# Kernel tuning notes

Hardware: AMD Instinct MI355X
Metric: run time of the kernel (lower is better)

## Reference

```python
import jax, jax.numpy as jnp
import numpy as np

B, N, T = 64, 256, 512          # batch, num_objs, num_triples
DO, DP, H, DOUT = 512, 512, 512, 512


def setup_inputs() -> dict:
    key = jax.random.key(0)
    ks = jax.random.split(key, 12)

    def kaiming(k, shape):
        fan_in = shape[0]
        return jax.random.normal(k, shape, jnp.float32) * np.sqrt(2.0 / fan_in)

    return {
        "obj_vecs": jax.random.normal(ks[0], (B, N, DO), jnp.float32),
        "pred_vecs": jax.random.normal(ks[1], (B, T, DP), jnp.float32),
        "edges": jax.random.randint(ks[2], (B, T, 3), 0, N, jnp.int64),
        # net1: [2*DO+DP -> H -> 2*H+DOUT], ReLU after each Linear
        "n1_w1": kaiming(ks[3], (2 * DO + DP, H)),
        "n1_b1": jnp.zeros((H,), jnp.float32),
        "n1_w2": kaiming(ks[4], (H, 2 * H + DOUT)),
        "n1_b2": jnp.zeros((2 * H + DOUT,), jnp.float32),
        # net2: [H -> H -> DOUT], ReLU after each Linear
        "n2_w1": kaiming(ks[5], (H, H)),
        "n2_b1": jnp.zeros((H,), jnp.float32),
        "n2_w2": kaiming(ks[6], (H, DOUT)),
        "n2_b2": jnp.zeros((DOUT,), jnp.float32),
    }


def reference(obj_vecs, pred_vecs, edges,
              n1_w1, n1_b1, n1_w2, n1_b2,
              n2_w1, n2_b1, n2_w2, n2_b2):
    num_batch, num_objs, _ = obj_vecs.shape
    h_dim = n1_b1.shape[0]
    d_out = n2_w2.shape[1]

    s_idx = edges[:, :, 0]            # [B, T] subject node ids
    o_idx = edges[:, :, 2]            # [B, T] object node ids

    # gather subject/object vectors per triple
    cur_s = jnp.take_along_axis(obj_vecs, s_idx[:, :, None], axis=1)  # [B,T,DO]
    cur_o = jnp.take_along_axis(obj_vecs, o_idx[:, :, None], axis=1)  # [B,T,DO]
    cur_t = jnp.concatenate([cur_s, pred_vecs, cur_o], axis=-1)       # [B,T,2DO+DP]

    # net1 MLP (Linear+ReLU, Linear+ReLU)
    hid = jax.nn.relu(jnp.einsum('btd,dh->bth', cur_t, n1_w1) + n1_b1)
    new_t = jax.nn.relu(jnp.einsum('bth,hk->btk', hid, n1_w2) + n1_b2)

    new_s = new_t[:, :, :h_dim]
    new_p = new_t[:, :, h_dim:h_dim + d_out]
    new_o = new_t[:, :, h_dim + d_out:2 * h_dim + d_out]

    # scatter-add back to nodes, per batch element
    b_ix = jnp.arange(num_batch)[:, None]            # [B,1]
    pooled = jnp.zeros((num_batch, num_objs, h_dim), obj_vecs.dtype)
    pooled = pooled.at[b_ix, s_idx].add(new_s)
    pooled = pooled.at[b_ix, o_idx].add(new_o)

    # avg pooling: divide by per-node incidence count (clamped at 1)
    ones = jnp.ones(s_idx.shape, obj_vecs.dtype)
    counts = jnp.zeros((num_batch, num_objs), obj_vecs.dtype)
    counts = counts.at[b_ix, s_idx].add(ones)
    counts = counts.at[b_ix, o_idx].add(ones)
    counts = jnp.maximum(counts, 1.0)
    pooled = pooled / counts[:, :, None]

    # net2 MLP (Linear+ReLU, Linear+ReLU)
    h2 = jax.nn.relu(jnp.einsum('bnh,hk->bnk', pooled, n2_w1) + n2_b1)
    new_obj_vecs = jax.nn.relu(jnp.einsum('bnh,hd->bnd', h2, n2_w2) + n2_b2)

    return new_obj_vecs, new_p
```

## Files before the change

kernel.cpp:

```cpp
#include <hip/hip_runtime.h>

typedef __bf16 bf16;
typedef __attribute__((ext_vector_type(2))) __bf16 bf16x2;
typedef __attribute__((ext_vector_type(4))) __bf16 bf16x4;
typedef __attribute__((ext_vector_type(8))) __bf16 bf16x8;
typedef __attribute__((ext_vector_type(4))) float f32x4;

#define DEVINL __device__ __forceinline__

typedef __attribute__((address_space(1))) void gvoid_t;
typedef __attribute__((address_space(3))) void lvoid_t;

DEVINL void async_ld16(const void* g, void* l) {
    __builtin_amdgcn_global_load_lds((gvoid_t*)g, (lvoid_t*)l, 16, 0, 0);
}

DEVINL void wait_vm0()   { asm volatile("s_waitcnt vmcnt(0)" ::: "memory"); }
DEVINL void wait_lgkm0() { asm volatile("s_waitcnt lgkmcnt(0)" ::: "memory");
                           __builtin_amdgcn_sched_barrier(0); }
DEVINL void barrier_()   { __builtin_amdgcn_s_barrier();
                           __builtin_amdgcn_sched_barrier(0); }

template<int MODE>
__global__ __launch_bounds__(512, 1) void gemm8_k(
    const bf16* __restrict__ A, const bf16* __restrict__ Bt,
    const float* __restrict__ bias, bf16* __restrict__ Dbf,
    float* __restrict__ Df, bf16* __restrict__ Dbf2,
    const int* __restrict__ edges, const bf16* __restrict__ obj,
    const bf16* __restrict__ pred, int K, int NBN)
{
    const int tid = threadIdx.x;
    const int id = blockIdx.x;
    const int bn = (id >> 3) % NBN;
    const int bm = (id & 7) + 8 * ((id >> 3) / NBN);

    __shared__ __align__(16) bf16 lds[8 * 8192];

    const int g_slot = tid & 7;
    const int row0 = tid >> 3;

    unsigned offS[4], offP[4], offO[4], offA[4], offB[4];
#pragma unroll
    for (int hi = 0; hi < 4; hi++) {
        int r = (hi >> 1) * 128 + (hi & 1) * 64 + row0;
        int gr = bm * 256 + r;
        if (MODE == 0) {
            int b = gr >> 9;
            int s = edges[gr * 3 + 0] & 255;
            int o = edges[gr * 3 + 2] & 255;
            offS[hi] = (unsigned)(b * 256 + s) * 512u;
            offP[hi] = (unsigned)gr * 512u;
            offO[hi] = (unsigned)(b * 256 + o) * 512u;
        } else {
            offA[hi] = (unsigned)gr * (unsigned)K;
        }
        offB[hi] = (unsigned)(bn * 256 + r) * (unsigned)K;
    }

    auto STAGE = [&](int tt, int kind) {
        bf16* ldst = lds + ((tt & 1) * 4 + kind) * 8192;
        int h = kind & 1;
#pragma unroll
        for (int i = 0; i < 2; i++) {
            int r = i * 64 + row0;
            int gsrc = g_slot ^ (r & 7);
            int hi = h * 2 + i;
            const bf16* gp;
            if (kind < 2) {
                if (MODE == 0) {
                    int region = tt >> 3;
                    unsigned col = (unsigned)((tt & 7) * 64 + gsrc * 8);
                    if (region == 0)      gp = obj + offS[hi] + col;
                    else if (region == 1) gp = pred + offP[hi] + col;
                    else                  gp = obj + offO[hi] + col;
                } else {
                    gp = A + offA[hi] + (unsigned)(tt * 64 + gsrc * 8);
                }
            } else {
                gp = Bt + offB[hi] + (unsigned)(tt * 64 + gsrc * 8);
            }
            async_ld16(gp, ldst + (tid + i * 512) * 8);
        }
    };

    f32x4 acc[8][4];
    const f32x4 zero4 = {0.f, 0.f, 0.f, 0.f};
#pragma unroll
    for (int i = 0; i < 8; i++)
#pragma unroll
        for (int j = 0; j < 4; j++) acc[i][j] = zero4;

    const int wave = tid >> 6, lane = tid & 63;
    const int wm = wave >> 2, wn = wave & 3;
    const int lq = lane >> 4, lr = lane & 15;

    bf16x8 bfr[4];
    bf16x8 af[4];

    auto LDB = [&](int tt, int ks) {
        const bf16* base = lds + ((tt & 1) * 4 + 2 + (wn >> 1)) * 8192;
#pragma unroll
        for (int n = 0; n < 4; n++) {
            int rr = (wn & 1) * 64 + n * 16 + lr;
            int g = (ks * 4 + lq) ^ (rr & 7);
            bfr[n] = *(const bf16x8*)(base + (rr * 8 + g) * 8);
        }
    };
    auto LDA = [&](int tt, int ks, int h) {
        const bf16* base = lds + ((tt & 1) * 4 + wm) * 8192;
#pragma unroll
        for (int mi = 0; mi < 4; mi++) {
            int rr = (h * 4 + mi) * 16 + lr;
            int g = (ks * 4 + lq) ^ (rr & 7);
            af[mi] = *(const bf16x8*)(base + (rr * 8 + g) * 8);
        }
    };
    auto MM = [&](int h) {
        __builtin_amdgcn_s_setprio(1);
#pragma unroll
        for (int mi = 0; mi < 4; mi++)
#pragma unroll
            for (int n = 0; n < 4; n++)
                acc[h * 4 + mi][n] = __builtin_amdgcn_mfma_f32_16x16x32_bf16(
                    bfr[n], af[mi], acc[h * 4 + mi][n], 0, 0, 0);
        __builtin_amdgcn_s_setprio(0);
        __builtin_amdgcn_sched_barrier(0);
    };

    STAGE(0, 0); STAGE(0, 1); STAGE(0, 2); STAGE(0, 3);
    wait_vm0();
    barrier_();

    const int NT = K >> 6;
    for (int t = 0; t < NT; ++t) {
        const bool pf = (t + 1 < NT);
        LDB(t, 0); LDA(t, 0, 0);
        if (pf) { STAGE(t + 1, 0); STAGE(t + 1, 1); }
        barrier_();
        wait_lgkm0();
        MM(0);
        barrier_();
        LDA(t, 0, 1);
        if (pf) { STAGE(t + 1, 2); STAGE(t + 1, 3); }
        barrier_();
        wait_lgkm0();
        MM(1);
        barrier_();
        LDB(t, 1); LDA(t, 1, 0);
        barrier_();
        wait_lgkm0();
        MM(0);
        barrier_();
        LDA(t, 1, 1);
        if (pf) wait_vm0();
        barrier_();
        wait_lgkm0();
        MM(1);
        barrier_();
    }

    const int rowbase = bm * 256 + wm * 128;
    const int cb0 = bn * 256 + wn * 64;
    const bool f32p = (MODE == 1) && (cb0 >= 512) && (cb0 < 1024);

    if (!f32p) {
        bf16* cw = lds + wave * 8192;
        bf16* outp; int cb;
        if (MODE == 1) {
            if (cb0 < 512) { outp = Dbf;  cb = cb0; }
            else           { outp = Dbf2; cb = cb0 - 1024; }
        } else { outp = Dbf; cb = cb0; }
#pragma unroll
        for (int ni = 0; ni < 4; ++ni) {
            const f32x4 bv = *(const f32x4*)(bias + cb0 + ni * 16 + lq * 4);
#pragma unroll
            for (int mi = 0; mi < 8; ++mi) {
                f32x4 v = acc[mi][ni];
                int row = mi * 16 + lr;
                int sl = (ni * 2 + (lq >> 1)) ^ (row & 7);
                bf16x4 o4;
#pragma unroll
                for (int r = 0; r < 4; r++) {
                    float x = v[r] + bv[r];
                    o4[r] = (bf16)(x > 0.f ? x : 0.f);
                }
                *(bf16x4*)(cw + row * 64 + sl * 8 + (lq & 1) * 4) = o4;
            }
        }
#pragma unroll
        for (int it = 0; it < 16; ++it) {
            int g = it * 64 + lane;
            int row = g >> 3, k = g & 7;
            bf16x8 v = *(const bf16x8*)(cw + row * 64 + ((k ^ (row & 7)) * 8));
            *(bf16x8*)(outp + (unsigned)(rowbase + row) * 512u + cb + k * 8) = v;
        }
    } else {
        float* cwf = (float*)(lds + wave * 8192);
        const int cbf = cb0 - 512;
#pragma unroll
        for (int mh = 0; mh < 2; ++mh) {
#pragma unroll
            for (int ni = 0; ni < 4; ++ni) {
                const f32x4 bv = *(const f32x4*)(bias + cb0 + ni * 16 + lq * 4);
#pragma unroll
                for (int mi2 = 0; mi2 < 4; ++mi2) {
                    f32x4 v = acc[mh * 4 + mi2][ni];
                    int row = mi2 * 16 + lr;
                    int s16 = ni * 4 + lq;
                    int sl = (s16 & 8) | ((s16 & 7) ^ (row & 7));
                    f32x4 x;
#pragma unroll
                    for (int r = 0; r < 4; r++) {
                        float tt = v[r] + bv[r];
                        x[r] = tt > 0.f ? tt : 0.f;
                    }
                    *(f32x4*)(cwf + row * 64 + sl * 4) = x;
                }
            }
#pragma unroll
            for (int it = 0; it < 16; ++it) {
                int flat = it * 64 + lane;
                int row = flat >> 4, k = flat & 15;
                int kk = (k & 8) | ((k & 7) ^ (row & 7));
                f32x4 v = *(const f32x4*)(cwf + row * 64 + kk * 4);
                *(f32x4*)(Df + (unsigned)(rowbase + mh * 64 + row) * 512u
                          + cbf + k * 4) = v;
            }
            if (mh == 0) wait_lgkm0();
        }
    }
}

template<int MODE, int NBN>
__global__ __launch_bounds__(256, 2) void gemm_k(
    const bf16* __restrict__ A, const bf16* __restrict__ Bt,
    const float* __restrict__ bias, bf16* __restrict__ Dbf,
    float* __restrict__ Df, int K)
{
    const int tid = threadIdx.x;
    const int id = blockIdx.x;
    const int bn = (id >> 3) % NBN;
    const int bm = (id & 7) + 8 * ((id >> 3) / NBN);

    __shared__ __align__(16) bf16 lds[2 * 128 * 64];
    bf16* ldsA = lds;
    bf16* ldsB = lds + 128 * 64;

    const int g_slot = tid & 7;
    const int row0 = tid >> 3;

    unsigned offA[4], offB[4];
#pragma unroll
    for (int i = 0; i < 4; i++) {
        int r = row0 + 32 * i;
        offA[i] = (unsigned)(bm * 128 + r) * (unsigned)K;
        offB[i] = (unsigned)(bn * 128 + r) * (unsigned)K;
    }

    f32x4 acc[4][4];
    const f32x4 zero4 = {0.f, 0.f, 0.f, 0.f};
#pragma unroll
    for (int i = 0; i < 4; i++)
#pragma unroll
        for (int j = 0; j < 4; j++) acc[i][j] = zero4;

    const int wave = tid >> 6;
    const int lane = tid & 63;
    const int wr = (wave >> 1) * 64;
    const int wc = (wave & 1) * 64;
    const int lq = lane >> 4;
    const int lr = lane & 15;

    const int KT = K >> 6;
    for (int kt = 0; kt < KT; ++kt) {
        __syncthreads();
#pragma unroll
        for (int i = 0; i < 4; i++) {
            int r = row0 + 32 * i;
            int gsrc = g_slot ^ (r & 7);
            async_ld16(A + offA[i] + (unsigned)(kt * 64 + gsrc * 8),
                       ldsA + (tid + i * 256) * 8);
        }
#pragma unroll
        for (int i = 0; i < 4; i++) {
            int r = row0 + 32 * i;
            int gsrc = g_slot ^ (r & 7);
            async_ld16(Bt + offB[i] + (unsigned)(kt * 64 + gsrc * 8),
                       ldsB + (tid + i * 256) * 8);
        }
        __syncthreads();

#pragma unroll
        for (int ks = 0; ks < 2; ++ks) {
            bf16x8 af[4], bfr[4];
#pragma unroll
            for (int mi = 0; mi < 4; ++mi) {
                int r = wr + mi * 16 + lr;
                int g = (ks * 4 + lq) ^ (r & 7);
                af[mi] = *(const bf16x8*)(ldsA + (r * 8 + g) * 8);
            }
#pragma unroll
            for (int ni = 0; ni < 4; ++ni) {
                int r = wc + ni * 16 + lr;
                int g = (ks * 4 + lq) ^ (r & 7);
                bfr[ni] = *(const bf16x8*)(ldsB + (r * 8 + g) * 8);
            }
#pragma unroll
            for (int mi = 0; mi < 4; ++mi)
#pragma unroll
                for (int ni = 0; ni < 4; ++ni)
                    acc[mi][ni] = __builtin_amdgcn_mfma_f32_16x16x32_bf16(
                        bfr[ni], af[mi], acc[mi][ni], 0, 0, 0);
        }
    }

    __syncthreads();
    const int rb = bm * 128 + wr;

    if (MODE == 2) {
        bf16* cw = lds + wave * 4096;
        const int cb = bn * 128 + wc;
#pragma unroll
        for (int ni = 0; ni < 4; ++ni) {
            const f32x4 bv = *(const f32x4*)(bias + cb + ni * 16 + lq * 4);
#pragma unroll
            for (int mi = 0; mi < 4; ++mi) {
                f32x4 v = acc[mi][ni];
                int row = mi * 16 + lr;
                int sl = (ni * 2 + (lq >> 1)) ^ (row & 7);
                bf16x4 o4;
#pragma unroll
                for (int r = 0; r < 4; r++) {
                    float t = v[r] + bv[r];
                    o4[r] = (bf16)(t > 0.f ? t : 0.f);
                }
                *(bf16x4*)(cw + row * 64 + sl * 8 + (lq & 1) * 4) = o4;
            }
        }
#pragma unroll
        for (int it = 0; it < 8; ++it) {
            int g = it * 64 + lane;
            int row = g >> 3, k = g & 7;
            bf16x8 v = *(const bf16x8*)(cw + row * 64 + ((k ^ (row & 7)) * 8));
            *(bf16x8*)(Dbf + (unsigned)(rb + row) * 512u + cb + k * 8) = v;
        }
    } else {
        float* cwf = (float*)lds + wave * 2048;
        const int cbf = bn * 128 + wc;
#pragma unroll
        for (int half = 0; half < 2; ++half) {
#pragma unroll
            for (int ni = 0; ni < 4; ++ni) {
                const f32x4 bv = *(const f32x4*)(bias + cbf + ni * 16 + lq * 4);
#pragma unroll
                for (int mi2 = 0; mi2 < 2; ++mi2) {
                    f32x4 v = acc[half * 2 + mi2][ni];
                    int row = mi2 * 16 + lr;
                    int s16 = ni * 4 + lq;
                    int sl = (s16 & 8) | ((s16 & 7) ^ (row & 7));
                    f32x4 x;
#pragma unroll
                    for (int r = 0; r < 4; r++) {
                        float t = v[r] + bv[r];
                        x[r] = t > 0.f ? t : 0.f;
                    }
                    *(f32x4*)(cwf + row * 64 + sl * 4) = x;
                }
            }
#pragma unroll
            for (int it = 0; it < 8; ++it) {
                int g = it * 64 + lane;
                int row = g >> 4, k = g & 15;
                int kk = (k & 8) | ((k & 7) ^ (row & 7));
                f32x4 v = *(const f32x4*)(cwf + row * 64 + kk * 4);
                *(f32x4*)(Df + (unsigned)(rb + half * 32 + row) * 512u + cbf + k * 4) = v;
            }
        }
    }
}

__global__ void pre_k(const float4* __restrict__ o, const float4* __restrict__ p,
                      bf16x4* __restrict__ ob, bf16x4* __restrict__ pb,
                      const float* __restrict__ w1, bf16* __restrict__ w1t,
                      const float* __restrict__ w2, bf16* __restrict__ w2t,
                      const float* __restrict__ w3, bf16* __restrict__ w3t,
                      const float* __restrict__ w4, bf16* __restrict__ w4t) {
    __shared__ float tile[32][33];
    int blk = blockIdx.x;
    int t = threadIdx.x;
    if (blk >= 24576) {
        int id = blk - 24576;
        const float* src; bf16* dst; int R, C, bx, by;
        if (id < 768)       { src = w1; dst = w1t; R = 1536; C = 512;  bx = id % 16; by = id / 16; }
        else if (id < 1536) { id -= 768;  src = w2; dst = w2t; R = 512; C = 1536; bx = id % 48; by = id / 48; }
        else if (id < 1792) { id -= 1536; src = w3; dst = w3t; R = 512; C = 512;  bx = id % 16; by = id / 16; }
        else                { id -= 1792; src = w4; dst = w4t; R = 512; C = 512;  bx = id % 16; by = id / 16; }
        int c0 = bx * 32, r0 = by * 32;
        int tx = t & 31, ty = t >> 5;
#pragma unroll
        for (int i = 0; i < 4; i++)
            tile[ty + i * 8][tx] = src[(size_t)(r0 + ty + i * 8) * C + c0 + tx];
        __syncthreads();
#pragma unroll
        for (int i = 0; i < 4; i++)
            dst[(size_t)(c0 + ty + i * 8) * R + r0 + tx] = (bf16)tile[tx][ty + i * 8];
        return;
    }
    int i = blk * 256 + t;
    if (i < 2097152) {
        float4 v = o[i];
        bf16x4 r = { (bf16)v.x, (bf16)v.y, (bf16)v.z, (bf16)v.w };
        ob[i] = r;
    } else {
        int j = i - 2097152;
        float4 v = p[j];
        bf16x4 r = { (bf16)v.x, (bf16)v.y, (bf16)v.z, (bf16)v.w };
        pb[j] = r;
    }
}

__global__ __launch_bounds__(256) void pool3_k(
    const int* __restrict__ edges,
    const bf16* __restrict__ new_s, const bf16* __restrict__ new_o,
    bf16* __restrict__ out)
{
    __shared__ int ent[1024];
    __shared__ int ec;
    const int idx = blockIdx.x;
    const int b = idx >> 8, n = idx & 255;
    const int t = threadIdx.x;
    if (t == 0) ec = 0;
    __syncthreads();
#pragma unroll
    for (int e0 = 0; e0 < 2; e0++) {
        int row = b * 512 + t + e0 * 256;
        int s = edges[row * 3 + 0] & 255;
        int o = edges[row * 3 + 2] & 255;
        if (s == n) { int ps = atomicAdd(&ec, 1); ent[ps] = row << 1; }
        if (o == n) { int po = atomicAdd(&ec, 1); ent[po] = (row << 1) | 1; }
    }
    __syncthreads();
    const int c = ec;
    float a0 = 0.f, a1 = 0.f, c0 = 0.f, c1 = 0.f;
    int j = 0;
    for (; j + 1 < c; j += 2) {
        int v0 = ent[j], v1 = ent[j + 1];
        const bf16x2* r0 = (const bf16x2*)(((v0 & 1) ? new_o : new_s) +
                                           (unsigned)(v0 >> 1) * 512u);
        const bf16x2* r1 = (const bf16x2*)(((v1 & 1) ? new_o : new_s) +
                                           (unsigned)(v1 >> 1) * 512u);
        bf16x2 w0 = r0[t];
        bf16x2 w1 = r1[t];
        a0 += (float)w0[0];
        a1 += (float)w0[1];
        c0 += (float)w1[0];
        c1 += (float)w1[1];
    }
    if (j < c) {
        int v = ent[j];
        const bf16x2* rp = (const bf16x2*)(((v & 1) ? new_o : new_s) +
                                           (unsigned)(v >> 1) * 512u);
        bf16x2 w = rp[t];
        a0 += (float)w[0];
        a1 += (float)w[1];
    }
    a0 += c0;
    a1 += c1;
    float inv = 1.f / (float)(c > 1 ? c : 1);
    bf16x2 o2 = { (bf16)(a0 * inv), (bf16)(a1 * inv) };
    *(bf16x2*)(out + (unsigned)idx * 512u + (unsigned)(t * 2)) = o2;
}

extern "C" void kernel_launch(void* const* d_in, const int* in_sizes, int n_in,
                              void* d_out, int out_size, void* d_ws, size_t ws_size,
                              hipStream_t stream) {
    const float* obj_f  = (const float*)d_in[0];
    const float* pred_f = (const float*)d_in[1];
    const int*   edges  = (const int*)d_in[2];
    const float* w1 = (const float*)d_in[3];
    const float* b1 = (const float*)d_in[4];
    const float* w2 = (const float*)d_in[5];
    const float* b2 = (const float*)d_in[6];
    const float* w3 = (const float*)d_in[7];
    const float* b3 = (const float*)d_in[8];
    const float* w4 = (const float*)d_in[9];
    const float* b4 = (const float*)d_in[10];

    char* ws = (char*)d_ws;
    bf16* obj_bf  = (bf16*)(ws + 0);
    bf16* pred_bf = (bf16*)(ws + 16777216);
    bf16* new_s   = (bf16*)(ws + 0);
    bf16* w1t = (bf16*)(ws + 50331648);
    bf16* w2t = (bf16*)(ws + 51904512);
    bf16* w3t = (bf16*)(ws + 53477376);
    bf16* w4t = (bf16*)(ws + 54001664);
    bf16* hid = (bf16*)(ws + 54525952);
    bf16* pooled_bf = hid;
    bf16* h2  = (bf16*)(ws + 71303168);

    float* out_obj = (float*)d_out;
    float* out_p   = (float*)d_out + 8388608;
    bf16* new_o    = (bf16*)d_out;

    pre_k<<<26624, 256, 0, stream>>>((const float4*)obj_f, (const float4*)pred_f,
                                     (bf16x4*)obj_bf, (bf16x4*)pred_bf,
                                     w1, w1t, w2, w2t, w3, w3t, w4, w4t);

    gemm8_k<0><<<256, 512, 0, stream>>>(
        nullptr, w1t, b1, hid, nullptr, nullptr, edges, obj_bf, pred_bf,
        1536, 2);

    gemm8_k<1><<<768, 512, 0, stream>>>(
        hid, w2t, b2, new_s, out_p, new_o, nullptr, nullptr, nullptr,
        512, 6);

    pool3_k<<<16384, 256, 0, stream>>>(edges, new_s, new_o, pooled_bf);

    gemm_k<2, 4><<<512, 256, 0, stream>>>(pooled_bf, w3t, b3, h2, nullptr, 512);

    gemm_k<3, 4><<<512, 256, 0, stream>>>(h2, w4t, b4, nullptr, out_obj, 512);
}
```

Baseline: 348.9 us.

## Fuse fp32-to-bf16 conversion of gathered inputs into first GEMM's A staging

Removes the separate pre-pass that converted obj_vecs and pred_vecs to bf16 in workspace. The first GEMM now loads fp32 rows directly into registers, converts them to bf16 and writes them to LDS, while the weight tiles keep using async global-to-LDS loads. This avoids writing and re-reading the bf16 copies, at the cost of more register pressure, twice the A-side global bytes per tile, and synchronous register-staged loads inside the pipelined loop.

```diff
diff --git a/kernel.cpp b/kernel.cpp
--- a/kernel.cpp
+++ b/kernel.cpp
@@ -26,8 +26,8 @@
     const bf16* __restrict__ A, const bf16* __restrict__ Bt,
     const float* __restrict__ bias, bf16* __restrict__ Dbf,
     float* __restrict__ Df, bf16* __restrict__ Dbf2,
-    const int* __restrict__ edges, const bf16* __restrict__ obj,
-    const bf16* __restrict__ pred, int K, int NBN)
+    const int* __restrict__ edges, const float* __restrict__ objf,
+    const float* __restrict__ predf, int K, int NBN)
 {
     const int tid = threadIdx.x;
     const int id = blockIdx.x;
@@ -67,19 +67,43 @@
             int hi = h * 2 + i;
             const bf16* gp;
             if (kind < 2) {
-                if (MODE == 0) {
-                    int region = tt >> 3;
-                    unsigned col = (unsigned)((tt & 7) * 64 + gsrc * 8);
-                    if (region == 0)      gp = obj + offS[hi] + col;
-                    else if (region == 1) gp = pred + offP[hi] + col;
-                    else                  gp = obj + offO[hi] + col;
-                } else {
-                    gp = A + offA[hi] + (unsigned)(tt * 64 + gsrc * 8);
-                }
+                gp = A + offA[hi] + (unsigned)(tt * 64 + gsrc * 8);
             } else {
                 gp = Bt + offB[hi] + (unsigned)(tt * 64 + gsrc * 8);
             }
             async_ld16(gp, ldst + (tid + i * 512) * 8);
+        }
+    };
+
+    float4 fA[8];
+    auto A_LOAD = [&](int tt, int kind) {
+#pragma unroll
+        for (int i = 0; i < 2; i++) {
+            int r = i * 64 + row0;
+            int gsrc = g_slot ^ (r & 7);
+            int hi = kind * 2 + i;
+            int region = tt >> 3;
+            unsigned col = (unsigned)((tt & 7) * 64 + gsrc * 8);
+            const float* gp;
+            if (region == 0)      gp = objf + offS[hi] + col;
+            else if (region == 1) gp = predf + offP[hi] + col;
+            else                  gp = objf + offO[hi] + col;
+            fA[kind * 4 + i * 2 + 0] = *(const float4*)gp;
+            fA[kind * 4 + i * 2 + 1] = *(const float4*)(gp + 4);
+        }
+    };
+    auto A_WRITE = [&](int tt, int kind) {
+        bf16* ldst = lds + ((tt & 1) * 4 + kind) * 8192;
+#pragma unroll
+        for (int i = 0; i < 2; i++) {
+            float4 v0 = fA[kind * 4 + i * 2 + 0];
+            float4 v1 = fA[kind * 4 + i * 2 + 1];
+            bf16x8 w;
+            w[0] = (bf16)v0.x; w[1] = (bf16)v0.y;
+            w[2] = (bf16)v0.z; w[3] = (bf16)v0.w;
+            w[4] = (bf16)v1.x; w[5] = (bf16)v1.y;
+            w[6] = (bf16)v1.z; w[7] = (bf16)v1.w;
+            *(bf16x8*)(ldst + (tid + i * 512) * 8) = w;
         }
     };
 
@@ -127,32 +151,50 @@
         __builtin_amdgcn_sched_barrier(0);
     };
 
-    STAGE(0, 0); STAGE(0, 1); STAGE(0, 2); STAGE(0, 3);
-    wait_vm0();
+    if (MODE == 0) {
+        STAGE(0, 2); STAGE(0, 3);
+        A_LOAD(0, 0); A_LOAD(0, 1);
+        wait_vm0();
+        A_WRITE(0, 0); A_WRITE(0, 1);
+        wait_lgkm0();
+    } else {
+        STAGE(0, 0); STAGE(0, 1); STAGE(0, 2); STAGE(0, 3);
+        wait_vm0();
+    }
     barrier_();
 
     const int NT = K >> 6;
     for (int t = 0; t < NT; ++t) {
         const bool pf = (t + 1 < NT);
         LDB(t, 0); LDA(t, 0, 0);
-        if (pf) { STAGE(t + 1, 0); STAGE(t + 1, 1); }
+        if (pf) {
+            if (MODE == 0) { STAGE(t + 1, 2); STAGE(t + 1, 3); }
+            else           { STAGE(t + 1, 0); STAGE(t + 1, 1); }
+        }
         barrier_();
         wait_lgkm0();
         MM(0);
         barrier_();
         LDA(t, 0, 1);
-        if (pf) { STAGE(t + 1, 2); STAGE(t + 1, 3); }
+        if (pf) {
+            if (MODE == 0) A_LOAD(t + 1, 0);
+            else           { STAGE(t + 1, 2); STAGE(t + 1, 3); }
+        }
         barrier_();
         wait_lgkm0();
         MM(1);
         barrier_();
         LDB(t, 1); LDA(t, 1, 0);
+        if (pf && MODE == 0) A_LOAD(t + 1, 1);
         barrier_();
         wait_lgkm0();
         MM(0);
         barrier_();
         LDA(t, 1, 1);
-        if (pf) wait_vm0();
+        if (pf) {
+            wait_vm0();
+            if (MODE == 0) { A_WRITE(t + 1, 0); A_WRITE(t + 1, 1); }
+        }
         barrier_();
         wait_lgkm0();
         MM(1);
@@ -379,44 +421,27 @@
     }
 }
 
-__global__ void pre_k(const float4* __restrict__ o, const float4* __restrict__ p,
-                      bf16x4* __restrict__ ob, bf16x4* __restrict__ pb,
-                      const float* __restrict__ w1, bf16* __restrict__ w1t,
+__global__ void pre_k(const float* __restrict__ w1, bf16* __restrict__ w1t,
                       const float* __restrict__ w2, bf16* __restrict__ w2t,
                       const float* __restrict__ w3, bf16* __restrict__ w3t,
                       const float* __restrict__ w4, bf16* __restrict__ w4t) {
     __shared__ float tile[32][33];
-    int blk = blockIdx.x;
+    int id = blockIdx.x;
     int t = threadIdx.x;
-    if (blk >= 24576) {
-        int id = blk - 24576;
-        const float* src; bf16* dst; int R, C, bx, by;
-        if (id < 768)       { src = w1; dst = w1t; R = 1536; C = 512;  bx = id % 16; by = id / 16; }
-        else if (id < 1536) { id -= 768;  src = w2; dst = w2t; R = 512; C = 1536; bx = id % 48; by = id / 48; }
-        else if (id < 1792) { id -= 1536; src = w3; dst = w3t; R = 512; C = 512;  bx = id % 16; by = id / 16; }
-        else                { id -= 1792; src = w4; dst = w4t; R = 512; C = 512;  bx = id % 16; by = id / 16; }
-        int c0 = bx * 32, r0 = by * 32;
-        int tx = t & 31, ty = t >> 5;
-#pragma unroll
-        for (int i = 0; i < 4; i++)
-            tile[ty + i * 8][tx] = src[(size_t)(r0 + ty + i * 8) * C + c0 + tx];
-        __syncthreads();
-#pragma unroll
-        for (int i = 0; i < 4; i++)
-            dst[(size_t)(c0 + ty + i * 8) * R + r0 + tx] = (bf16)tile[tx][ty + i * 8];
-        return;
-    }
-    int i = blk * 256 + t;
-    if (i < 2097152) {
-        float4 v = o[i];
-        bf16x4 r = { (bf16)v.x, (bf16)v.y, (bf16)v.z, (bf16)v.w };
-        ob[i] = r;
-    } else {
-        int j = i - 2097152;
-        float4 v = p[j];
-        bf16x4 r = { (bf16)v.x, (bf16)v.y, (bf16)v.z, (bf16)v.w };
-        pb[j] = r;
-    }
+    const float* src; bf16* dst; int R, C, bx, by;
+    if (id < 768)       { src = w1; dst = w1t; R = 1536; C = 512;  bx = id % 16; by = id / 16; }
+    else if (id < 1536) { id -= 768;  src = w2; dst = w2t; R = 512; C = 1536; bx = id % 48; by = id / 48; }
+    else if (id < 1792) { id -= 1536; src = w3; dst = w3t; R = 512; C = 512;  bx = id % 16; by = id / 16; }
+    else                { id -= 1792; src = w4; dst = w4t; R = 512; C = 512;  bx = id % 16; by = id / 16; }
+    int c0 = bx * 32, r0 = by * 32;
+    int tx = t & 31, ty = t >> 5;
+#pragma unroll
+    for (int i = 0; i < 4; i++)
+        tile[ty + i * 8][tx] = src[(size_t)(r0 + ty + i * 8) * C + c0 + tx];
+    __syncthreads();
+#pragma unroll
+    for (int i = 0; i < 4; i++)
+        dst[(size_t)(c0 + ty + i * 8) * R + r0 + tx] = (bf16)tile[tx][ty + i * 8];
 }
 
 __global__ __launch_bounds__(256) void pool3_k(
@@ -487,8 +512,6 @@
     const float* b4 = (const float*)d_in[10];
 
     char* ws = (char*)d_ws;
-    bf16* obj_bf  = (bf16*)(ws + 0);
-    bf16* pred_bf = (bf16*)(ws + 16777216);
     bf16* new_s   = (bf16*)(ws + 0);
     bf16* w1t = (bf16*)(ws + 50331648);
     bf16* w2t = (bf16*)(ws + 51904512);
@@ -502,12 +525,10 @@
     float* out_p   = (float*)d_out + 8388608;
     bf16* new_o    = (bf16*)d_out;
 
-    pre_k<<<26624, 256, 0, stream>>>((const float4*)obj_f, (const float4*)pred_f,
-                                     (bf16x4*)obj_bf, (bf16x4*)pred_bf,
-                                     w1, w1t, w2, w2t, w3, w3t, w4, w4t);
+    pre_k<<<2048, 256, 0, stream>>>(w1, w1t, w2, w2t, w3, w3t, w4, w4t);
 
     gemm8_k<0><<<256, 512, 0, stream>>>(
-        nullptr, w1t, b1, hid, nullptr, nullptr, edges, obj_bf, pred_bf,
+        nullptr, w1t, b1, hid, nullptr, nullptr, edges, obj_f, pred_f,
         1536, 2);
 
     gemm8_k<1><<<768, 512, 0, stream>>>(
```

After: 348.6 us. No clear change (-0.1%).
